# Kernel tuning notes

Measured on AMD Instinct MI355X. Metric: run time of the kernel, lower is better.

The kernel has to match this reference:

```python
import jax, jax.numpy as jnp
import numpy as np
import math

N = 16384
IN_F = 256
OUT_F = 64
EPS = 1e-6


def setup_inputs() -> dict:
    key = jax.random.key(0)
    k1, k2, k3, k4 = jax.random.split(key, 4)
    stdv = 1.0 / math.sqrt(OUT_F)
    inp = jax.random.normal(k1, (N, IN_F), dtype=jnp.float32)
    adj = jax.random.uniform(k2, (N, N), dtype=jnp.float32)
    weight = jax.random.uniform(k3, (IN_F, OUT_F), dtype=jnp.float32, minval=-stdv, maxval=stdv)
    bias = jax.random.uniform(k4, (OUT_F,), dtype=jnp.float32, minval=-stdv, maxval=stdv)
    return {"input": inp, "adj": adj, "weight": weight, "bias": bias, "p": 2}


def reference(input, adj, weight, bias, p):
    # support: [N, OUT_F]
    support = input @ weight
    mu = jnp.min(support)  # global scalar min
    pre_sup = support - mu + EPS  # >= EPS, safe for pow
    pre_top = pre_sup ** (p + 1)
    pre_down = pre_sup ** p
    # p-power mean aggregation: two adj matmuls sharing adj reads
    output = (adj @ pre_top) / (adj @ pre_down) + mu
    return output + bias
```

## Files before the change

kernel.cpp:

```cpp
#include <hip/hip_runtime.h>
#include <hip/hip_bf16.h>

typedef __attribute__((ext_vector_type(8))) short short8;
typedef __attribute__((ext_vector_type(4))) float f32x4;
typedef unsigned short u16;
typedef unsigned int u32;

#define NROWS 16384
#define KDIM 16384
#define EPS 1e-6f

__device__ __forceinline__ u16 f2bf(float x) {
    union { float f; u32 u; } v; v.f = x;
    u32 u = v.u;
    u32 r = (u + 0x7FFFu + ((u >> 16) & 1u)) >> 16;
    return (u16)r;
}

__device__ __forceinline__ void glds16(const void* g, void* l) {
    __builtin_amdgcn_global_load_lds(
        (const __attribute__((address_space(1))) void*)g,
        (__attribute__((address_space(3))) void*)l, 16, 0, 0);
}

__device__ __forceinline__ short cvbf(float x) {
    __hip_bfloat16 h = __float2bfloat16(x);
    return *(short*)&h;
}

__global__ __launch_bounds__(256) void wt_kernel(const float* __restrict__ W,
                                                 float* __restrict__ Wt) {
    int idx = blockIdx.x * 256 + threadIdx.x;
    int k = idx >> 6, c = idx & 63;
    Wt[c * 256 + k] = W[idx];
}

__global__ __launch_bounds__(256) void support_kernel(
    const float* __restrict__ inp, const float* __restrict__ Wt,
    float* __restrict__ sup)
{
    int tid = threadIdx.x;
    int col = tid & 63;
    int rr = tid >> 6;
    int rowbase = blockIdx.x * 32 + rr * 8;
    const float4* wt4 = (const float4*)(Wt + (size_t)col * 256);
    float acc[8];
#pragma unroll
    for (int i = 0; i < 8; ++i) acc[i] = 0.f;
    for (int k4 = 0; k4 < 64; ++k4) {
        float4 wv = wt4[k4];
#pragma unroll
        for (int i = 0; i < 8; ++i) {
            float4 iv = *((const float4*)(inp + (size_t)(rowbase + i) * 256) + k4);
            acc[i] += iv.x * wv.x + iv.y * wv.y + iv.z * wv.z + iv.w * wv.w;
        }
    }
#pragma unroll
    for (int i = 0; i < 8; ++i)
        sup[(size_t)(rowbase + i) * 64 + col] = acc[i];
}

__global__ __launch_bounds__(256) void min_part_kernel(
    const float* __restrict__ sup, float* __restrict__ partmin)
{
    __shared__ float wmin[4];
    int tid = threadIdx.x;
    const float4* s4 = (const float4*)sup;
    size_t idx = (size_t)blockIdx.x * 256 + tid;
    float m = 3.4e38f;
#pragma unroll
    for (int j = 0; j < 4; ++j) {
        float4 v = s4[idx + (size_t)j * 65536];
        m = fminf(m, fminf(fminf(v.x, v.y), fminf(v.z, v.w)));
    }
#pragma unroll
    for (int off = 32; off; off >>= 1) m = fminf(m, __shfl_down(m, off, 64));
    if ((tid & 63) == 0) wmin[tid >> 6] = m;
    __syncthreads();
    if (tid == 0)
        partmin[blockIdx.x] = fminf(fminf(wmin[0], wmin[1]), fminf(wmin[2], wmin[3]));
}

__global__ __launch_bounds__(256) void min_final_kernel(
    const float* __restrict__ partmin, float* __restrict__ mu)
{
    __shared__ float wmin[4];
    int tid = threadIdx.x;
    float m = partmin[tid];
#pragma unroll
    for (int off = 32; off; off >>= 1) m = fminf(m, __shfl_down(m, off, 64));
    if ((tid & 63) == 0) wmin[tid >> 6] = m;
    __syncthreads();
    if (tid == 0)
        mu[0] = fminf(fminf(wmin[0], wmin[1]), fminf(wmin[2], wmin[3]));
}

__global__ __launch_bounds__(256) void build_bt_kernel(
    const float* __restrict__ sup, const float* __restrict__ muptr,
    const int* __restrict__ pptr, u16* __restrict__ Bt)
{
    int k = blockIdx.x * 256 + threadIdx.x;
    float mu = *muptr;
    int p = *pptr;
    const float4* srow = (const float4*)(sup + (size_t)k * 64);
#pragma unroll
    for (int j = 0; j < 16; ++j) {
        float4 v = srow[j];
        float ss[4] = {v.x, v.y, v.z, v.w};
#pragma unroll
        for (int q = 0; q < 4; ++q) {
            int c = j * 4 + q;
            float s = ss[q] - mu + EPS;
            float d = 1.f;
            for (int i = 0; i < p; ++i) d *= s;
            Bt[(size_t)c * KDIM + k] = f2bf(d * s);
            Bt[(size_t)(c + 64) * KDIM + k] = f2bf(d);
        }
    }
}

#define BM 64
#define BN 128
#define BK 64
#define KH 8192
#define NTI 128

__global__ __launch_bounds__(512, 4) void gemm_kernel(
    const float* __restrict__ adj, const u16* __restrict__ Bt,
    float* __restrict__ Pp)
{
    __shared__ __align__(16) u16 Ash[2][BM * BK];
    __shared__ __align__(16) u16 Bsh[2][BN * BK];

    const int tid = threadIdx.x;
    const int P = blockIdx.x;
    const int L = (P & 7) * 64 + (P >> 3);
    const int h  = L >> 8;
    const int rb = L & 255;
    const size_t rowbase = (size_t)rb * BM;
    const size_t kbase   = (size_t)h * KH;

    const int ars = tid >> 3;
    const int ac8 = tid & 7;
    const float* asrc = adj + (rowbase + ars) * KDIM + kbase + ac8 * 8;
    const int awoff = ars * 8 + (ac8 ^ (ars & 7));

    const int ga0 = tid, ga1 = tid + 512;
    const int bn0 = ga0 >> 3, bx0 = (ga0 & 7) ^ (bn0 & 7);
    const int bn1 = ga1 >> 3, bx1 = (ga1 & 7) ^ (bn1 & 7);
    const u16* bsrc0 = Bt + (size_t)bn0 * KDIM + kbase + bx0 * 8;
    const u16* bsrc1 = Bt + (size_t)bn1 * KDIM + kbase + bx1 * 8;

    const int lane = tid & 63;
    const int w    = tid >> 6;
    const int wm   = w >> 2;
    const int wn   = w & 3;
    const int l15  = lane & 15, lg = lane >> 4;
    const int arow0 = wm * 32 + l15;
    const int arow1 = arow0 + 16;
    const int nt = wn * 16 + l15;
    const int nd = nt + 64;
    const int asw = arow0 & 7;
    const int bsw = nt & 7;

    f32x4 acc00 = {0.f, 0.f, 0.f, 0.f};
    f32x4 acc01 = acc00, acc10 = acc00, acc11 = acc00;

    float4 ra0, ra1;

    auto issueA = [&](int kt) {
        const float4* ap = (const float4*)(asrc + kt * BK);
        ra0 = ap[0]; ra1 = ap[1];
    };
    auto issueB = [&](int kt, int buf) {
        char* bb = (char*)Bsh[buf];
        const int koff = kt * BK;
        glds16(bsrc0 + koff, bb + ga0 * 16);
        glds16(bsrc1 + koff, bb + ga1 * 16);
    };
    auto writeA = [&](int buf) {
        uint4 awv;
        awv.x = (u32)(u16)cvbf(ra0.x) | ((u32)(u16)cvbf(ra0.y) << 16);
        awv.y = (u32)(u16)cvbf(ra0.z) | ((u32)(u16)cvbf(ra0.w) << 16);
        awv.z = (u32)(u16)cvbf(ra1.x) | ((u32)(u16)cvbf(ra1.y) << 16);
        awv.w = (u32)(u16)cvbf(ra1.z) | ((u32)(u16)cvbf(ra1.w) << 16);
        ((uint4*)Ash[buf])[awoff] = awv;
    };

    issueA(0);
    issueB(0, 0);
    writeA(0);

    for (int t = 0; t < NTI; ++t) {
        __syncthreads();
        const int nb = (t + 1) & 1;
        if (t + 1 < NTI) {
            issueA(t + 1);
            issueB(t + 1, nb);
        }
        const short8* As8 = (const short8*)Ash[t & 1];
        const short8* Bs8 = (const short8*)Bsh[t & 1];
#pragma unroll
        for (int ks = 0; ks < 2; ++ks) {
            const int g = ks * 4 + lg;
            short8 a0 = As8[arow0 * 8 + (g ^ asw)];
            short8 a1 = As8[arow1 * 8 + (g ^ asw)];
            short8 b0 = Bs8[nt * 8 + (g ^ bsw)];
            short8 b1 = Bs8[nd * 8 + (g ^ bsw)];
            acc00 = __builtin_amdgcn_mfma_f32_16x16x32_bf16(a0, b0, acc00, 0, 0, 0);
            acc01 = __builtin_amdgcn_mfma_f32_16x16x32_bf16(a0, b1, acc01, 0, 0, 0);
            acc10 = __builtin_amdgcn_mfma_f32_16x16x32_bf16(a1, b0, acc10, 0, 0, 0);
            acc11 = __builtin_amdgcn_mfma_f32_16x16x32_bf16(a1, b1, acc11, 0, 0, 0);
        }
        if (t + 1 < NTI) writeA(nb);
    }

    float* pb = Pp + (size_t)L * (BM * BN);
#pragma unroll
    for (int q = 0; q < 4; ++q) {
        int r0 = wm * 32 + lg * 4 + q;
        int r1 = r0 + 16;
        pb[r0 * BN + nt] = acc00[q];
        pb[r0 * BN + nd] = acc01[q];
        pb[r1 * BN + nt] = acc10[q];
        pb[r1 * BN + nd] = acc11[q];
    }
}

__global__ __launch_bounds__(256) void reduce_kernel(
    const float* __restrict__ Pp, const float* __restrict__ bias,
    const float* __restrict__ muptr, float* __restrict__ out)
{
    int idx = blockIdx.x * 256 + threadIdx.x;
    int r = idx >> 6, c = idx & 63;
    int rb = r >> 6, rr = r & 63;
    const float* p0 = Pp + (size_t)rb * (BM * BN) + rr * BN + c;
    const float* p1 = p0 + (size_t)256 * (BM * BN);
    float T = p0[0]  + p1[0];
    float D = p0[64] + p1[64];
    out[idx] = T / D + muptr[0] + bias[c];
}

extern "C" void kernel_launch(void* const* d_in, const int* in_sizes, int n_in,
                              void* d_out, int out_size, void* d_ws, size_t ws_size,
                              hipStream_t stream)
{
    const float* inp  = (const float*)d_in[0];
    const float* adj  = (const float*)d_in[1];
    const float* W    = (const float*)d_in[2];
    const float* bias = (const float*)d_in[3];
    const int*   p    = (const int*)d_in[4];
    float* out = (float*)d_out;

    char* ws = (char*)d_ws;
    u16*   Bt      = (u16*)ws;
    float* partmin = (float*)(ws + (size_t)4 * 1024 * 1024);
    float* mu      = partmin + 256;
    float* Wt      = (float*)(ws + (size_t)4 * 1024 * 1024 + 4096);
    float* Pp      = (float*)(ws + (size_t)8 * 1024 * 1024);

    float* sup = out;

    wt_kernel       <<<64,   256, 0, stream>>>(W, Wt);
    support_kernel  <<<512,  256, 0, stream>>>(inp, Wt, sup);
    min_part_kernel <<<256,  256, 0, stream>>>(sup, partmin);
    min_final_kernel<<<1,    256, 0, stream>>>(partmin, mu);
    build_bt_kernel <<<64,   256, 0, stream>>>(sup, mu, p, Bt);
    gemm_kernel     <<<512,  512, 0, stream>>>(adj, Bt, Pp);
    reduce_kernel   <<<4096, 256, 0, stream>>>(Pp, bias, mu, out);
}
```

Before: 327.2 us.

## Prefetch A two tiles ahead with unrolled double-buffer loop and simpler block mapping

The main loop is unrolled by two so each half has its own named register set for the A prefetch. A loads now run two k-tiles ahead of the bf16 convert-and-store into LDS, and the B async LDS load is issued before compute. The block-to-tile mapping drops the XCD-style swizzle: adjacent blocks now take the two K-halves of the same row block, and the partial-sum layout and reduce kernel are changed to match. This adds register pressure and alters L2/XCD locality, and either could hurt.

```diff
diff --git a/kernel.cpp b/kernel.cpp
--- a/kernel.cpp
+++ b/kernel.cpp
@@ -133,17 +133,14 @@
     __shared__ __align__(16) u16 Bsh[2][BN * BK];
 
     const int tid = threadIdx.x;
-    const int P = blockIdx.x;
-    const int L = (P & 7) * 64 + (P >> 3);
-    const int h  = L >> 8;
-    const int rb = L & 255;
+    const int rb = blockIdx.x >> 1;
+    const int h  = blockIdx.x & 1;
     const size_t rowbase = (size_t)rb * BM;
     const size_t kbase   = (size_t)h * KH;
 
-    const int ars = tid >> 3;
-    const int ac8 = tid & 7;
-    const float* asrc = adj + (rowbase + ars) * KDIM + kbase + ac8 * 8;
-    const int awoff = ars * 8 + (ac8 ^ (ars & 7));
+    const int ar = tid >> 3, ac = tid & 7;
+    const float* asrc = adj + (rowbase + ar) * KDIM + kbase + ac * 8;
+    const int awslot = ar * 8 + (ac ^ (ar & 7));
 
     const int ga0 = tid, ga1 = tid + 512;
     const int bn0 = ga0 >> 3, bx0 = (ga0 & 7) ^ (bn0 & 7);
@@ -158,71 +155,79 @@
     const int l15  = lane & 15, lg = lane >> 4;
     const int arow0 = wm * 32 + l15;
     const int arow1 = arow0 + 16;
-    const int nt = wn * 16 + l15;
-    const int nd = nt + 64;
-    const int asw = arow0 & 7;
-    const int bsw = nt & 7;
+    const int asw   = arow0 & 7;
+    const int n0    = wn * 16 + l15;
+    const int nd    = n0 + 64;
+    const int bsw   = n0 & 7;
 
     f32x4 acc00 = {0.f, 0.f, 0.f, 0.f};
     f32x4 acc01 = acc00, acc10 = acc00, acc11 = acc00;
 
-    float4 ra0, ra1;
-
-    auto issueA = [&](int kt) {
-        const float4* ap = (const float4*)(asrc + kt * BK);
-        ra0 = ap[0]; ra1 = ap[1];
-    };
-    auto issueB = [&](int kt, int buf) {
+    auto gldsB = [&](int kt, int buf) {
         char* bb = (char*)Bsh[buf];
         const int koff = kt * BK;
         glds16(bsrc0 + koff, bb + ga0 * 16);
         glds16(bsrc1 + koff, bb + ga1 * 16);
     };
-    auto writeA = [&](int buf) {
-        uint4 awv;
-        awv.x = (u32)(u16)cvbf(ra0.x) | ((u32)(u16)cvbf(ra0.y) << 16);
-        awv.y = (u32)(u16)cvbf(ra0.z) | ((u32)(u16)cvbf(ra0.w) << 16);
-        awv.z = (u32)(u16)cvbf(ra1.x) | ((u32)(u16)cvbf(ra1.y) << 16);
-        awv.w = (u32)(u16)cvbf(ra1.z) | ((u32)(u16)cvbf(ra1.w) << 16);
-        ((uint4*)Ash[buf])[awoff] = awv;
-    };
-
-    issueA(0);
-    issueB(0, 0);
-    writeA(0);
-
-    for (int t = 0; t < NTI; ++t) {
-        __syncthreads();
-        const int nb = (t + 1) & 1;
-        if (t + 1 < NTI) {
-            issueA(t + 1);
-            issueB(t + 1, nb);
-        }
-        const short8* As8 = (const short8*)Ash[t & 1];
-        const short8* Bs8 = (const short8*)Bsh[t & 1];
+    auto loadA = [&](int kt, float4& x, float4& y) {
+        const float4* p = (const float4*)(asrc + kt * BK);
+        x = p[0]; y = p[1];
+    };
+    auto writeA = [&](const float4& x, const float4& y, int buf) {
+        uint4 v;
+        v.x = (u32)(u16)cvbf(x.x) | ((u32)(u16)cvbf(x.y) << 16);
+        v.y = (u32)(u16)cvbf(x.z) | ((u32)(u16)cvbf(x.w) << 16);
+        v.z = (u32)(u16)cvbf(y.x) | ((u32)(u16)cvbf(y.y) << 16);
+        v.w = (u32)(u16)cvbf(y.z) | ((u32)(u16)cvbf(y.w) << 16);
+        ((uint4*)Ash[buf])[awslot] = v;
+    };
+    auto compute = [&](int buf) {
+        const short8* As8 = (const short8*)Ash[buf];
+        const short8* Bs8 = (const short8*)Bsh[buf];
 #pragma unroll
         for (int ks = 0; ks < 2; ++ks) {
             const int g = ks * 4 + lg;
             short8 a0 = As8[arow0 * 8 + (g ^ asw)];
             short8 a1 = As8[arow1 * 8 + (g ^ asw)];
-            short8 b0 = Bs8[nt * 8 + (g ^ bsw)];
-            short8 b1 = Bs8[nd * 8 + (g ^ bsw)];
-            acc00 = __builtin_amdgcn_mfma_f32_16x16x32_bf16(a0, b0, acc00, 0, 0, 0);
-            acc01 = __builtin_amdgcn_mfma_f32_16x16x32_bf16(a0, b1, acc01, 0, 0, 0);
-            acc10 = __builtin_amdgcn_mfma_f32_16x16x32_bf16(a1, b0, acc10, 0, 0, 0);
-            acc11 = __builtin_amdgcn_mfma_f32_16x16x32_bf16(a1, b1, acc11, 0, 0, 0);
+            short8 bt_ = Bs8[n0 * 8 + (g ^ bsw)];
+            short8 bd_ = Bs8[nd * 8 + (g ^ bsw)];
+            acc00 = __builtin_amdgcn_mfma_f32_16x16x32_bf16(a0, bt_, acc00, 0, 0, 0);
+            acc01 = __builtin_amdgcn_mfma_f32_16x16x32_bf16(a0, bd_, acc01, 0, 0, 0);
+            acc10 = __builtin_amdgcn_mfma_f32_16x16x32_bf16(a1, bt_, acc10, 0, 0, 0);
+            acc11 = __builtin_amdgcn_mfma_f32_16x16x32_bf16(a1, bd_, acc11, 0, 0, 0);
         }
-        if (t + 1 < NTI) writeA(nb);
-    }
-
-    float* pb = Pp + (size_t)L * (BM * BN);
+    };
+
+    float4 pa0, pa1;
+    float4 pb0, pb1;
+
+    loadA(0, pa0, pa1);
+    gldsB(0, 0);
+    writeA(pa0, pa1, 0);
+    loadA(1, pa0, pa1);
+    __syncthreads();
+
+    for (int tt = 0; tt < NTI; tt += 2) {
+        if (tt + 1 < NTI) gldsB(tt + 1, 1);
+        if (tt + 2 < NTI) loadA(tt + 2, pb0, pb1);
+        compute(0);
+        if (tt + 1 < NTI) writeA(pa0, pa1, 1);
+        __syncthreads();
+        if (tt + 2 < NTI) gldsB(tt + 2, 0);
+        if (tt + 3 < NTI) loadA(tt + 3, pa0, pa1);
+        compute(1);
+        if (tt + 2 < NTI) writeA(pb0, pb1, 0);
+        __syncthreads();
+    }
+
+    float* pb = Pp + (size_t)blockIdx.x * (BM * BN);
 #pragma unroll
     for (int q = 0; q < 4; ++q) {
         int r0 = wm * 32 + lg * 4 + q;
         int r1 = r0 + 16;
-        pb[r0 * BN + nt] = acc00[q];
+        pb[r0 * BN + n0] = acc00[q];
         pb[r0 * BN + nd] = acc01[q];
-        pb[r1 * BN + nt] = acc10[q];
+        pb[r1 * BN + n0] = acc10[q];
         pb[r1 * BN + nd] = acc11[q];
     }
 }
@@ -234,8 +239,8 @@
     int idx = blockIdx.x * 256 + threadIdx.x;
     int r = idx >> 6, c = idx & 63;
     int rb = r >> 6, rr = r & 63;
-    const float* p0 = Pp + (size_t)rb * (BM * BN) + rr * BN + c;
-    const float* p1 = p0 + (size_t)256 * (BM * BN);
+    const float* p0 = Pp + (size_t)(rb * 2) * (BM * BN) + rr * BN + c;
+    const float* p1 = p0 + BM * BN;
     float T = p0[0]  + p1[0];
     float D = p0[64] + p1[64];
     out[idx] = T / D + muptr[0] + bias[c];
```

Result: faster. 291.0 us (-11.1%).
